# Performance work log

Measured on AMD Instinct MI355X. Metric: run time of the kernel, lower is better.

Reference implementation:

```python
import jax, jax.numpy as jnp
import numpy as np

NUM_BLOCKS = 8
D = 1024          # residual_dim == attention_dim
FF = 4096         # feed_forward_dim
B, S = 4, 4096
EPS_ATTN = 1e-6
EPS_LN = 1e-6


def _ln(x, scale, bias):
    m = jnp.mean(x, axis=-1, keepdims=True)
    v = jnp.var(x, axis=-1, keepdims=True)
    return (x - m) * jax.lax.rsqrt(v + EPS_LN) * scale + bias


def setup_inputs() -> dict:
    key = jax.random.key(0)
    ks = jax.random.split(key, 16)
    g = lambda k, shape, fan: jax.random.normal(k, shape, jnp.float32) * (1.0 / np.sqrt(fan))
    inp = {
        "x": jax.random.normal(ks[0], (B, S, D), jnp.float32),
        "Wq": g(ks[1], (NUM_BLOCKS, D, D), D), "bq": jnp.zeros((NUM_BLOCKS, D), jnp.float32),
        "Wk": g(ks[2], (NUM_BLOCKS, D, D), D), "bk": jnp.zeros((NUM_BLOCKS, D), jnp.float32),
        "Wv": g(ks[3], (NUM_BLOCKS, D, D), D), "bv": jnp.zeros((NUM_BLOCKS, D), jnp.float32),
        "Wo": g(ks[4], (NUM_BLOCKS, D, D), D), "bo": jnp.zeros((NUM_BLOCKS, D), jnp.float32),
        "ln1_s": jnp.ones((NUM_BLOCKS, D), jnp.float32), "ln1_b": jnp.zeros((NUM_BLOCKS, D), jnp.float32),
        "W1": g(ks[5], (NUM_BLOCKS, D, FF), D), "b1": jnp.zeros((NUM_BLOCKS, FF), jnp.float32),
        "W2": g(ks[6], (NUM_BLOCKS, FF, D), FF), "b2": jnp.zeros((NUM_BLOCKS, D), jnp.float32),
        "ln2_s": jnp.ones((NUM_BLOCKS, D), jnp.float32), "ln2_b": jnp.zeros((NUM_BLOCKS, D), jnp.float32),
    }
    return inp


def _forward(x, Wq, bq, Wk, bk, Wv, bv, Wo, bo, ln1_s, ln1_b, W1, b1, W2, b2, ln2_s, ln2_b):
    gelu = lambda t: jax.nn.gelu(t, approximate=True)  # flax nn.gelu default
    fmap = lambda t: jax.nn.elu(t) + 1.0
    for i in range(NUM_BLOCKS):
        # --- linear attention sublayer ---
        residual = x
        Q = fmap(x @ Wq[i] + bq[i])          # [b, s, h]
        K = fmap(x @ Wk[i] + bk[i])          # [b, s, h]
        value = x @ Wv[i] + bv[i]            # [b, s, h]
        KV = jnp.einsum('nsh,nsh->nh', K, value)          # per-channel sum_s K*V
        Ksum = jnp.sum(K, axis=1)                         # [b, h]
        Z = 1.0 / (Q * Ksum[:, None, :] + EPS_ATTN)       # [b, s, h]
        V = Q * KV[:, None, :] * Z                        # [b, s, h]
        attn_out = gelu(V @ Wo[i] + bo[i])
        x = _ln(attn_out + residual, ln1_s[i], ln1_b[i])
        # --- feed-forward sublayer ---
        residual = x
        h = gelu(x @ W1[i] + b1[i])
        ff_out = gelu(h @ W2[i] + b2[i])
        x = _ln(ff_out + residual, ln2_s[i], ln2_b[i])
    return x


def reference(x, Wq, bq, Wk, bk, Wv, bv, Wo, bo, ln1_s, ln1_b, W1, b1, W2, b2, ln2_s, ln2_b):
    return _forward(x, Wq, bq, Wk, bk, Wv, bv, Wo, bo, ln1_s, ln1_b, W1, b1, W2, b2, ln2_s, ln2_b)
```

## Files before the change

### kernel.cpp

```cpp
#include <hip/hip_runtime.h>
#include <hip/hip_bf16.h>
#include <cstdint>

typedef unsigned short ushort_t;
typedef __attribute__((ext_vector_type(8))) short short8;
typedef __attribute__((ext_vector_type(4))) float floatx4;
typedef __attribute__((ext_vector_type(4))) ushort_t ushort4v;

#define DEVI __device__ __forceinline__

DEVI float b2f(ushort_t u){ union{unsigned int i; float f;} v; v.i = ((unsigned int)u)<<16; return v.f; }
DEVI ushort_t f2b(float f){ union{float f; unsigned int i;} v; v.f=f; unsigned int r = (v.i + 0x7FFFu + ((v.i>>16)&1u)) >> 16; return (ushort_t)r; }

DEVI float gelu_f(float t){
  float t3 = t*t*t;
  return 0.5f*t*(1.0f + tanhf(0.7978845608028654f*(t + 0.044715f*t3)));
}

#define GLD_LDS16(src, dst) \
  __builtin_amdgcn_global_load_lds((const __attribute__((address_space(1))) void*)(src), \
                                   (__attribute__((address_space(3))) void*)(dst), 16, 0, 0)

template<int EPI>
__global__ __launch_bounds__(256)
void gemm_kernel(const ushort_t* __restrict__ A, const ushort_t* __restrict__ Bt,
                 const float* __restrict__ bias, const float* __restrict__ res,
                 ushort_t* __restrict__ out, int N, int K)
{
  __shared__ alignas(16) ushort_t As[2][4096];
  __shared__ alignas(16) ushort_t Bs[2][4096];
  const int tid  = threadIdx.x;
  const int wave = tid >> 6, lane = tid & 63;
  const int quad = lane >> 4, l16 = lane & 15;
  const int tileM = blockIdx.x * 128, tileN = blockIdx.y * 128;
  const int wm = (wave >> 1) * 64, wn = (wave & 1) * 64;
  const int sw = quad ^ (l16 & 3);

  floatx4 acc[4][4] = {};

  const int r0 = tid >> 2,        kd0 = (tid & 3) ^ (r0 & 3);
  const int r1 = (256+tid) >> 2,  kd1 = ((256+tid) & 3) ^ (r1 & 3);
  const size_t aoff0 = (size_t)(tileM + r0) * K + kd0 * 8;
  const size_t aoff1 = (size_t)(tileM + r1) * K + kd1 * 8;
  const size_t boff0 = (size_t)(tileN + r0) * K + kd0 * 8;
  const size_t boff1 = (size_t)(tileN + r1) * K + kd1 * 8;

  GLD_LDS16(A  + aoff0, &As[0][0] + wave*512);
  GLD_LDS16(A  + aoff1, &As[0][0] + 2048 + wave*512);
  GLD_LDS16(Bt + boff0, &Bs[0][0] + wave*512);
  GLD_LDS16(Bt + boff1, &Bs[0][0] + 2048 + wave*512);

  const int nIter = K >> 5;
  for (int it = 0; it < nIter; ++it){
    const int cur = it & 1, nxt = cur ^ 1;
    __syncthreads();
    if (it + 1 < nIter){
      const size_t k8 = (size_t)(it + 1) * 32;
      GLD_LDS16(A  + aoff0 + k8, &As[nxt][0] + wave*512);
      GLD_LDS16(A  + aoff1 + k8, &As[nxt][0] + 2048 + wave*512);
      GLD_LDS16(Bt + boff0 + k8, &Bs[nxt][0] + wave*512);
      GLD_LDS16(Bt + boff1 + k8, &Bs[nxt][0] + 2048 + wave*512);
    }
    short8 af[4], bfv[4];
    #pragma unroll
    for (int i = 0; i < 4; i++){
      af[i]  = *(const short8*)(&As[cur][0] + ((wm + i*16 + l16)*4 + sw)*8);
      bfv[i] = *(const short8*)(&Bs[cur][0] + ((wn + i*16 + l16)*4 + sw)*8);
    }
    #pragma unroll
    for (int mi = 0; mi < 4; mi++)
      #pragma unroll
      for (int ni = 0; ni < 4; ni++)
        acc[mi][ni] = __builtin_amdgcn_mfma_f32_16x16x32_bf16(af[mi], bfv[ni], acc[mi][ni], 0, 0, 0);
  }

  float bv4[4];
  #pragma unroll
  for (int ni = 0; ni < 4; ni++) bv4[ni] = bias[tileN + wn + ni*16 + l16];

  #pragma unroll
  for (int mi = 0; mi < 4; mi++){
    #pragma unroll
    for (int r = 0; r < 4; r++){
      const int row = tileM + wm + mi*16 + quad*4 + r;
      #pragma unroll
      for (int ni = 0; ni < 4; ni++){
        const int col = tileN + wn + ni*16 + l16;
        float v = acc[mi][ni][r] + bv4[ni];
        if constexpr (EPI == 0){ v = (v > 0.f) ? (v + 1.f) : expf(v); }
        else if constexpr (EPI == 2){ v = gelu_f(v); }
        else if constexpr (EPI == 3){ v = gelu_f(v) + res[(size_t)row*N + col]; }
        out[(size_t)row*N + col] = f2b(v);
      }
    }
  }
}

__global__ __launch_bounds__(256)
void qkv_gemm_kernel(const ushort_t* __restrict__ A, const ushort_t* __restrict__ Bt,
                     const float* __restrict__ bq, const float* __restrict__ bk,
                     const float* __restrict__ bv,
                     ushort_t* __restrict__ outQ, ushort_t* __restrict__ outK,
                     ushort_t* __restrict__ outV, int K)
{
  __shared__ alignas(16) ushort_t As[2][4096];
  __shared__ alignas(16) ushort_t Bs[2][4096];
  const int tid  = threadIdx.x;
  const int wave = tid >> 6, lane = tid & 63;
  const int quad = lane >> 4, l16 = lane & 15;
  const int tileM = blockIdx.x * 128, tileN = blockIdx.y * 128;
  const int wm = (wave >> 1) * 64, wn = (wave & 1) * 64;
  const int sw = quad ^ (l16 & 3);

  const int seg = tileN >> 10;
  const int nloc = tileN & 1023;
  const float* bias = (seg == 0) ? bq : (seg == 1) ? bk : bv;
  ushort_t* out     = (seg == 0) ? outQ : (seg == 1) ? outK : outV;

  floatx4 acc[4][4] = {};

  const int r0 = tid >> 2,        kd0 = (tid & 3) ^ (r0 & 3);
  const int r1 = (256+tid) >> 2,  kd1 = ((256+tid) & 3) ^ (r1 & 3);
  const size_t aoff0 = (size_t)(tileM + r0) * K + kd0 * 8;
  const size_t aoff1 = (size_t)(tileM + r1) * K + kd1 * 8;
  const size_t boff0 = (size_t)(tileN + r0) * K + kd0 * 8;
  const size_t boff1 = (size_t)(tileN + r1) * K + kd1 * 8;

  GLD_LDS16(A  + aoff0, &As[0][0] + wave*512);
  GLD_LDS16(A  + aoff1, &As[0][0] + 2048 + wave*512);
  GLD_LDS16(Bt + boff0, &Bs[0][0] + wave*512);
  GLD_LDS16(Bt + boff1, &Bs[0][0] + 2048 + wave*512);

  const int nIter = K >> 5;
  for (int it = 0; it < nIter; ++it){
    const int cur = it & 1, nxt = cur ^ 1;
    __syncthreads();
    if (it + 1 < nIter){
      const size_t k8 = (size_t)(it + 1) * 32;
      GLD_LDS16(A  + aoff0 + k8, &As[nxt][0] + wave*512);
      GLD_LDS16(A  + aoff1 + k8, &As[nxt][0] + 2048 + wave*512);
      GLD_LDS16(Bt + boff0 + k8, &Bs[nxt][0] + wave*512);
      GLD_LDS16(Bt + boff1 + k8, &Bs[nxt][0] + 2048 + wave*512);
    }
    short8 af[4], bfv[4];
    #pragma unroll
    for (int i = 0; i < 4; i++){
      af[i]  = *(const short8*)(&As[cur][0] + ((wm + i*16 + l16)*4 + sw)*8);
      bfv[i] = *(const short8*)(&Bs[cur][0] + ((wn + i*16 + l16)*4 + sw)*8);
    }
    #pragma unroll
    for (int mi = 0; mi < 4; mi++)
      #pragma unroll
      for (int ni = 0; ni < 4; ni++)
        acc[mi][ni] = __builtin_amdgcn_mfma_f32_16x16x32_bf16(af[mi], bfv[ni], acc[mi][ni], 0, 0, 0);
  }

  float bv4[4];
  #pragma unroll
  for (int ni = 0; ni < 4; ni++) bv4[ni] = bias[nloc + wn + ni*16 + l16];

  #pragma unroll
  for (int mi = 0; mi < 4; mi++){
    #pragma unroll
    for (int r = 0; r < 4; r++){
      const int row = tileM + wm + mi*16 + quad*4 + r;
      #pragma unroll
      for (int ni = 0; ni < 4; ni++){
        const int col = nloc + wn + ni*16 + l16;
        float v = acc[mi][ni][r] + bv4[ni];
        if (seg < 2){ v = (v > 0.f) ? (v + 1.f) : expf(v); }
        out[(size_t)row*1024 + col] = f2b(v);
      }
    }
  }
}

__global__ __launch_bounds__(256)
void reduce_kv_kernel(const ushort_t* __restrict__ Kb, const ushort_t* __restrict__ Vb,
                      float* __restrict__ KV, float* __restrict__ Ksum)
{
  const int b = blockIdx.x >> 6, chunk = blockIdx.x & 63;
  const int t = threadIdx.x;
  const size_t base = ((size_t)b*4096 + (size_t)chunk*64)*1024 + t*4;
  float kv[4] = {0,0,0,0}, ks[4] = {0,0,0,0};
  for (int s = 0; s < 64; s++){
    ushort4v kk = *(const ushort4v*)(Kb + base + (size_t)s*1024);
    ushort4v vv = *(const ushort4v*)(Vb + base + (size_t)s*1024);
    #pragma unroll
    for (int j = 0; j < 4; j++){ float kf = b2f(kk[j]); kv[j] += kf*b2f(vv[j]); ks[j] += kf; }
  }
  #pragma unroll
  for (int j = 0; j < 4; j++){
    atomicAdd(&KV[b*1024 + t*4 + j], kv[j]);
    atomicAdd(&Ksum[b*1024 + t*4 + j], ks[j]);
  }
}

__global__ __launch_bounds__(256)
void attn_map_kernel(ushort_t* __restrict__ Q, const float* __restrict__ KV, const float* __restrict__ Ksum)
{
  const size_t g = (size_t)blockIdx.x*256 + threadIdx.x;
  const size_t base = g*4;
  const int b  = (int)(base >> 22);
  const int h0 = (int)(base & 1023);
  ushort4v q4 = *(const ushort4v*)(Q + base);
  ushort4v o4;
  #pragma unroll
  for (int j = 0; j < 4; j++){
    float q = b2f(q4[j]);
    float v = q*KV[b*1024 + h0 + j] / (q*Ksum[b*1024 + h0 + j] + 1e-6f);
    o4[j] = f2b(v);
  }
  *(ushort4v*)(Q + base) = o4;
}

__global__ __launch_bounds__(256)
void ln_kernel(const ushort_t* __restrict__ y, const float* __restrict__ sc,
               const float* __restrict__ bi, ushort_t* __restrict__ xb, float* __restrict__ xf)
{
  const int row = blockIdx.x, t = threadIdx.x;
  const ushort_t* yr = y + (size_t)row*1024;
  ushort4v v4 = *(const ushort4v*)(yr + t*4);
  float f[4]; float s1 = 0.f, s2 = 0.f;
  #pragma unroll
  for (int j = 0; j < 4; j++){ f[j] = b2f(v4[j]); s1 += f[j]; s2 += f[j]*f[j]; }
  #pragma unroll
  for (int off = 32; off; off >>= 1){ s1 += __shfl_down(s1, off); s2 += __shfl_down(s2, off); }
  __shared__ float red[2][4];
  const int wave = t >> 6, lane = t & 63;
  if (lane == 0){ red[0][wave] = s1; red[1][wave] = s2; }
  __syncthreads();
  s1 = red[0][0] + red[0][1] + red[0][2] + red[0][3];
  s2 = red[1][0] + red[1][1] + red[1][2] + red[1][3];
  const float mean = s1 * (1.0f/1024.0f);
  const float var  = s2 * (1.0f/1024.0f) - mean*mean;
  const float inv  = rsqrtf(var + 1e-6f);
  ushort4v o4;
  #pragma unroll
  for (int j = 0; j < 4; j++){
    const int h = t*4 + j;
    const float o = (f[j] - mean)*inv*sc[h] + bi[h];
    o4[j] = f2b(o);
    xf[(size_t)row*1024 + h] = o;
  }
  *(ushort4v*)(xb + (size_t)row*1024 + t*4) = o4;
}

struct TParams { const float* src[6]; ushort_t* dst[6]; };

__global__ __launch_bounds__(256)
void transpose_all_kernel(TParams p)
{
  __shared__ float tile[32][33];
  const int id = blockIdx.x;
  int m, bx, by, R, C;
  if (id < 4096){ m = 4; int l = id;        bx = l & 127; by = l >> 7; R = 1024; C = 4096; }
  else if (id < 8192){ m = 5; int l = id - 4096; bx = l & 31; by = l >> 5; R = 4096; C = 1024; }
  else { int l = id - 8192; m = l >> 10; l &= 1023; bx = l & 31; by = l >> 5; R = 1024; C = 1024; }
  const float* in = p.src[m];
  ushort_t* out = p.dst[m];
  const int t = threadIdx.x;
  const int tx = t & 31, ty = t >> 5;
  const int rb = by*32, cb = bx*32;
  #pragma unroll
  for (int j = 0; j < 32; j += 8) tile[ty+j][tx] = in[(size_t)(rb+ty+j)*C + cb+tx];
  __syncthreads();
  #pragma unroll
  for (int j = 0; j < 32; j += 8) out[(size_t)(cb+ty+j)*R + rb+tx] = f2b(tile[tx][ty+j]);
}

__global__ __launch_bounds__(256)
void cvt_kernel(const float* __restrict__ in, ushort_t* __restrict__ out)
{
  const size_t base = ((size_t)blockIdx.x*256 + threadIdx.x)*4;
  ushort4v o4;
  #pragma unroll
  for (int j = 0; j < 4; j++) o4[j] = f2b(in[base + j]);
  *(ushort4v*)(out + base) = o4;
}

extern "C" void kernel_launch(void* const* d_in, const int* in_sizes, int n_in,
                              void* d_out, int out_size, void* d_ws, size_t ws_size,
                              hipStream_t stream)
{
  const float* x_in = (const float*)d_in[0];
  const float* Wq   = (const float*)d_in[1];
  const float* bq   = (const float*)d_in[2];
  const float* Wk   = (const float*)d_in[3];
  const float* bk   = (const float*)d_in[4];
  const float* Wv   = (const float*)d_in[5];
  const float* bv   = (const float*)d_in[6];
  const float* Wo   = (const float*)d_in[7];
  const float* bo   = (const float*)d_in[8];
  const float* ln1s = (const float*)d_in[9];
  const float* ln1b = (const float*)d_in[10];
  const float* W1   = (const float*)d_in[11];
  const float* b1   = (const float*)d_in[12];
  const float* W2   = (const float*)d_in[13];
  const float* b2   = (const float*)d_in[14];
  const float* ln2s = (const float*)d_in[15];
  const float* ln2b = (const float*)d_in[16];

  float* xf = (float*)d_out;

  char* ws = (char*)d_ws;
  const size_t MB = 1024*1024;
  ushort_t* xb     = (ushort_t*)(ws);
  char*     regB   = ws + 32*MB;
  ushort_t* bufQ   = (ushort_t*)(regB);
  ushort_t* bufK   = (ushort_t*)(regB + 32*MB);
  ushort_t* bufVal = (ushort_t*)(regB + 64*MB);
  ushort_t* bufH   = (ushort_t*)(regB);
  ushort_t* bufY   = (ushort_t*)(regB + 128*MB);
  ushort_t* WqkvT  = (ushort_t*)(ws + 192*MB);
  ushort_t* WoT    = (ushort_t*)(ws + 198*MB);
  ushort_t* W1T    = (ushort_t*)(ws + 200*MB);
  ushort_t* W2T    = (ushort_t*)(ws + 208*MB);
  float*    KV     = (float*)(ws + 216*MB);
  float*    Ksum   = (float*)(ws + 216*MB + 16*1024);

  const int M = 16384, D = 1024, FF = 4096;
  const dim3 blk(256);

  hipMemcpyAsync(xf, x_in, (size_t)M*D*sizeof(float), hipMemcpyDeviceToDevice, stream);
  cvt_kernel<<<dim3(M*D/1024), blk, 0, stream>>>(x_in, xb);

  for (int i = 0; i < 8; i++){
    TParams tp;
    tp.src[0] = Wq + (size_t)i*D*D;  tp.dst[0] = WqkvT;
    tp.src[1] = Wk + (size_t)i*D*D;  tp.dst[1] = WqkvT + 1024*1024;
    tp.src[2] = Wv + (size_t)i*D*D;  tp.dst[2] = WqkvT + 2*1024*1024;
    tp.src[3] = Wo + (size_t)i*D*D;  tp.dst[3] = WoT;
    tp.src[4] = W1 + (size_t)i*D*FF; tp.dst[4] = W1T;
    tp.src[5] = W2 + (size_t)i*FF*D; tp.dst[5] = W2T;
    transpose_all_kernel<<<dim3(12288), blk, 0, stream>>>(tp);

    qkv_gemm_kernel<<<dim3(128, 24), blk, 0, stream>>>(xb, WqkvT, bq + i*D, bk + i*D, bv + i*D,
                                                       bufQ, bufK, bufVal, D);

    hipMemsetAsync(KV, 0, 32*1024, stream);
    reduce_kv_kernel<<<dim3(256), blk, 0, stream>>>(bufK, bufVal, KV, Ksum);
    attn_map_kernel<<<dim3(16384), blk, 0, stream>>>(bufQ, KV, Ksum);

    gemm_kernel<3><<<dim3(128, 8), blk, 0, stream>>>(bufQ, WoT, bo + i*D, xf, bufVal, D, D);
    ln_kernel<<<dim3(16384), blk, 0, stream>>>(bufVal, ln1s + i*D, ln1b + i*D, xb, xf);

    gemm_kernel<2><<<dim3(128, 32), blk, 0, stream>>>(xb, W1T, b1 + i*FF, nullptr, bufH, FF, D);
    gemm_kernel<3><<<dim3(128, 8),  blk, 0, stream>>>(bufH, W2T, b2 + i*D, xf, bufY, D, FF);
    ln_kernel<<<dim3(16384), blk, 0, stream>>>(bufY, ln2s + i*D, ln2b + i*D, xb, xf);
  }
  (void)in_sizes; (void)n_in; (void)out_size; (void)ws_size;
}
```

Measured before the change: 6.651 ms.

## Use 256x256 GEMM tiles with 8 waves, BK=64 and split-phase pipelined loads

Replaces the 128x128, 4-wave, BK=32 GEMM mainloop with a shared 256x256, 8-wave core that uses 64-wide K steps and an XOR-swizzled LDS layout. Global-to-LDS loads are staged in pieces interleaved with MFMA phases, using explicit vmcnt waits, barriers and s_setprio to overlap memory with compute. The larger tile raises operand reuse and cuts global traffic per FLOP. In exchange it uses 128KB of LDS and more registers per block. The grid is smaller, so small GEMMs such as N=1024 get only 256 blocks, which can underfill the GPU.

```diff
diff --git a/kernel.cpp b/kernel.cpp
--- a/kernel.cpp
+++ b/kernel.cpp
@@ -21,155 +21,168 @@
   __builtin_amdgcn_global_load_lds((const __attribute__((address_space(1))) void*)(src), \
                                    (__attribute__((address_space(3))) void*)(dst), 16, 0, 0)
 
+#define BAR()    asm volatile("s_barrier" ::: "memory")
+#define WAITV(n) asm volatile("s_waitcnt vmcnt(" #n ")" ::: "memory")
+
+DEVI void gemm_core(const ushort_t* __restrict__ A, const ushort_t* __restrict__ Bt,
+                    int K, int tileM, int tileN, floatx4 (&acc)[8][4])
+{
+  __shared__ alignas(16) ushort_t As[2][16384];
+  __shared__ alignas(16) ushort_t Bs[2][16384];
+  const int tid  = threadIdx.x;
+  const int wave = tid >> 6, lane = tid & 63;
+  const int quad = lane >> 4, l16 = lane & 15;
+  const int wm = wave >> 2, wn = wave & 3;
+
+  const int rr = tid >> 3;
+  const int gg = (tid & 7) ^ (rr & 7);
+  const ushort_t* srcA = A  + (size_t)(tileM + rr) * K + gg * 8;
+  const ushort_t* srcB = Bt + (size_t)(tileN + rr) * K + gg * 8;
+  const size_t K64 = (size_t)K * 64;
+  ushort_t* dstA = &As[0][0] + wave * 512;
+  ushort_t* dstB = &Bs[0][0] + wave * 512;
+
+#define STAGE_R(t, r) do{ \
+    const ushort_t* s_ = (((r) < 2) ? srcA : srcB) + (size_t)(t) * 64 + (((r) & 1) ? 2*K64 : (size_t)0); \
+    ushort_t* d_ = (((r) < 2) ? dstA : dstB) + (((t) & 1) ? 16384 : 0) + (((r) & 1) ? 8192 : 0); \
+    GLD_LDS16(s_,       d_); \
+    GLD_LDS16(s_ + K64, d_ + 4096); \
+  }while(0)
+
+#define PHASE_MFMA(n0, n1) \
+    BAR(); \
+    __builtin_amdgcn_s_setprio(1); \
+    _Pragma("unroll") \
+    for (int mi = 0; mi < 8; mi++){ \
+      acc[mi][n0] = __builtin_amdgcn_mfma_f32_16x16x32_bf16(af[mi], bf0, acc[mi][n0], 0, 0, 0); \
+      acc[mi][n1] = __builtin_amdgcn_mfma_f32_16x16x32_bf16(af[mi], bf1, acc[mi][n1], 0, 0, 0); \
+    } \
+    __builtin_amdgcn_s_setprio(0); \
+    BAR()
+
+  const int nkt = K >> 6;
+  STAGE_R(0, 0); STAGE_R(0, 1); STAGE_R(0, 2); STAGE_R(0, 3);
+  if (nkt > 1){
+    STAGE_R(1, 0); STAGE_R(1, 1); STAGE_R(1, 2);
+    WAITV(6);
+  } else {
+    WAITV(0);
+  }
+  BAR();
+
+  const int s0   = (quad ^ (l16 & 7)) * 8;
+  const int aRow = (wm * 128 + l16) * 64;
+  const int bRow = (wn * 64  + l16) * 64;
+
+  for (int t = 0; t < nkt; ++t){
+    const ushort_t* as = &As[t & 1][0];
+    const ushort_t* bs = &Bs[t & 1][0];
+    if (t + 1 < nkt) STAGE_R(t + 1, 3);
+
+    short8 af[8], bf0, bf1;
+    #pragma unroll
+    for (int mi = 0; mi < 8; mi++) af[mi] = *(const short8*)(as + aRow + mi * 1024 + s0);
+    bf0 = *(const short8*)(bs + bRow + s0);
+    bf1 = *(const short8*)(bs + bRow + 1024 + s0);
+    PHASE_MFMA(0, 1);
+    bf0 = *(const short8*)(bs + bRow + 2 * 1024 + s0);
+    bf1 = *(const short8*)(bs + bRow + 3 * 1024 + s0);
+    PHASE_MFMA(2, 3);
+    {
+      const int s1 = s0 ^ 32;
+      #pragma unroll
+      for (int mi = 0; mi < 8; mi++) af[mi] = *(const short8*)(as + aRow + mi * 1024 + s1);
+      bf0 = *(const short8*)(bs + bRow + s1);
+      bf1 = *(const short8*)(bs + bRow + 1024 + s1);
+      PHASE_MFMA(0, 1);
+      bf0 = *(const short8*)(bs + bRow + 2 * 1024 + s1);
+      bf1 = *(const short8*)(bs + bRow + 3 * 1024 + s1);
+      PHASE_MFMA(2, 3);
+    }
+    if (t + 2 < nkt){
+      STAGE_R(t + 2, 0); STAGE_R(t + 2, 1); STAGE_R(t + 2, 2);
+      WAITV(6);
+      BAR();
+    } else if (t + 1 < nkt){
+      WAITV(0);
+      BAR();
+    }
+  }
+#undef STAGE_R
+#undef PHASE_MFMA
+}
+
 template<int EPI>
-__global__ __launch_bounds__(256)
+__global__ __launch_bounds__(512, 2)
 void gemm_kernel(const ushort_t* __restrict__ A, const ushort_t* __restrict__ Bt,
                  const float* __restrict__ bias, const float* __restrict__ res,
                  ushort_t* __restrict__ out, int N, int K)
 {
-  __shared__ alignas(16) ushort_t As[2][4096];
-  __shared__ alignas(16) ushort_t Bs[2][4096];
-  const int tid  = threadIdx.x;
-  const int wave = tid >> 6, lane = tid & 63;
+  const int tileM = blockIdx.x * 256, tileN = blockIdx.y * 256;
+  floatx4 acc[8][4] = {};
+  gemm_core(A, Bt, K, tileM, tileN, acc);
+
+  const int tid = threadIdx.x, wave = tid >> 6, lane = tid & 63;
   const int quad = lane >> 4, l16 = lane & 15;
-  const int tileM = blockIdx.x * 128, tileN = blockIdx.y * 128;
-  const int wm = (wave >> 1) * 64, wn = (wave & 1) * 64;
-  const int sw = quad ^ (l16 & 3);
-
-  floatx4 acc[4][4] = {};
-
-  const int r0 = tid >> 2,        kd0 = (tid & 3) ^ (r0 & 3);
-  const int r1 = (256+tid) >> 2,  kd1 = ((256+tid) & 3) ^ (r1 & 3);
-  const size_t aoff0 = (size_t)(tileM + r0) * K + kd0 * 8;
-  const size_t aoff1 = (size_t)(tileM + r1) * K + kd1 * 8;
-  const size_t boff0 = (size_t)(tileN + r0) * K + kd0 * 8;
-  const size_t boff1 = (size_t)(tileN + r1) * K + kd1 * 8;
-
-  GLD_LDS16(A  + aoff0, &As[0][0] + wave*512);
-  GLD_LDS16(A  + aoff1, &As[0][0] + 2048 + wave*512);
-  GLD_LDS16(Bt + boff0, &Bs[0][0] + wave*512);
-  GLD_LDS16(Bt + boff1, &Bs[0][0] + 2048 + wave*512);
-
-  const int nIter = K >> 5;
-  for (int it = 0; it < nIter; ++it){
-    const int cur = it & 1, nxt = cur ^ 1;
-    __syncthreads();
-    if (it + 1 < nIter){
-      const size_t k8 = (size_t)(it + 1) * 32;
-      GLD_LDS16(A  + aoff0 + k8, &As[nxt][0] + wave*512);
-      GLD_LDS16(A  + aoff1 + k8, &As[nxt][0] + 2048 + wave*512);
-      GLD_LDS16(Bt + boff0 + k8, &Bs[nxt][0] + wave*512);
-      GLD_LDS16(Bt + boff1 + k8, &Bs[nxt][0] + 2048 + wave*512);
-    }
-    short8 af[4], bfv[4];
-    #pragma unroll
-    for (int i = 0; i < 4; i++){
-      af[i]  = *(const short8*)(&As[cur][0] + ((wm + i*16 + l16)*4 + sw)*8);
-      bfv[i] = *(const short8*)(&Bs[cur][0] + ((wn + i*16 + l16)*4 + sw)*8);
-    }
-    #pragma unroll
-    for (int mi = 0; mi < 4; mi++)
-      #pragma unroll
-      for (int ni = 0; ni < 4; ni++)
-        acc[mi][ni] = __builtin_amdgcn_mfma_f32_16x16x32_bf16(af[mi], bfv[ni], acc[mi][ni], 0, 0, 0);
-  }
+  const int wm = wave >> 2, wn = wave & 3;
 
   float bv4[4];
   #pragma unroll
-  for (int ni = 0; ni < 4; ni++) bv4[ni] = bias[tileN + wn + ni*16 + l16];
-
-  #pragma unroll
-  for (int mi = 0; mi < 4; mi++){
+  for (int ni = 0; ni < 4; ni++) bv4[ni] = bias[tileN + wn * 64 + ni * 16 + l16];
+
+  #pragma unroll
+  for (int mi = 0; mi < 8; mi++){
     #pragma unroll
     for (int r = 0; r < 4; r++){
-      const int row = tileM + wm + mi*16 + quad*4 + r;
+      const int row = tileM + wm * 128 + mi * 16 + quad * 4 + r;
       #pragma unroll
       for (int ni = 0; ni < 4; ni++){
-        const int col = tileN + wn + ni*16 + l16;
+        const int col = tileN + wn * 64 + ni * 16 + l16;
         float v = acc[mi][ni][r] + bv4[ni];
         if constexpr (EPI == 0){ v = (v > 0.f) ? (v + 1.f) : expf(v); }
         else if constexpr (EPI == 2){ v = gelu_f(v); }
-        else if constexpr (EPI == 3){ v = gelu_f(v) + res[(size_t)row*N + col]; }
-        out[(size_t)row*N + col] = f2b(v);
+        else if constexpr (EPI == 3){ v = gelu_f(v) + res[(size_t)row * N + col]; }
+        out[(size_t)row * N + col] = f2b(v);
       }
     }
   }
 }
 
-__global__ __launch_bounds__(256)
+__global__ __launch_bounds__(512, 2)
 void qkv_gemm_kernel(const ushort_t* __restrict__ A, const ushort_t* __restrict__ Bt,
                      const float* __restrict__ bq, const float* __restrict__ bk,
                      const float* __restrict__ bv,
                      ushort_t* __restrict__ outQ, ushort_t* __restrict__ outK,
                      ushort_t* __restrict__ outV, int K)
 {
-  __shared__ alignas(16) ushort_t As[2][4096];
-  __shared__ alignas(16) ushort_t Bs[2][4096];
-  const int tid  = threadIdx.x;
-  const int wave = tid >> 6, lane = tid & 63;
+  const int tileM = blockIdx.x * 256, tileN = blockIdx.y * 256;
+  floatx4 acc[8][4] = {};
+  gemm_core(A, Bt, K, tileM, tileN, acc);
+
+  const int tid = threadIdx.x, wave = tid >> 6, lane = tid & 63;
   const int quad = lane >> 4, l16 = lane & 15;
-  const int tileM = blockIdx.x * 128, tileN = blockIdx.y * 128;
-  const int wm = (wave >> 1) * 64, wn = (wave & 1) * 64;
-  const int sw = quad ^ (l16 & 3);
-
-  const int seg = tileN >> 10;
+  const int wm = wave >> 2, wn = wave & 3;
+
+  const int seg  = tileN >> 10;
   const int nloc = tileN & 1023;
   const float* bias = (seg == 0) ? bq : (seg == 1) ? bk : bv;
   ushort_t* out     = (seg == 0) ? outQ : (seg == 1) ? outK : outV;
 
-  floatx4 acc[4][4] = {};
-
-  const int r0 = tid >> 2,        kd0 = (tid & 3) ^ (r0 & 3);
-  const int r1 = (256+tid) >> 2,  kd1 = ((256+tid) & 3) ^ (r1 & 3);
-  const size_t aoff0 = (size_t)(tileM + r0) * K + kd0 * 8;
-  const size_t aoff1 = (size_t)(tileM + r1) * K + kd1 * 8;
-  const size_t boff0 = (size_t)(tileN + r0) * K + kd0 * 8;
-  const size_t boff1 = (size_t)(tileN + r1) * K + kd1 * 8;
-
-  GLD_LDS16(A  + aoff0, &As[0][0] + wave*512);
-  GLD_LDS16(A  + aoff1, &As[0][0] + 2048 + wave*512);
-  GLD_LDS16(Bt + boff0, &Bs[0][0] + wave*512);
-  GLD_LDS16(Bt + boff1, &Bs[0][0] + 2048 + wave*512);
-
-  const int nIter = K >> 5;
-  for (int it = 0; it < nIter; ++it){
-    const int cur = it & 1, nxt = cur ^ 1;
-    __syncthreads();
-    if (it + 1 < nIter){
-      const size_t k8 = (size_t)(it + 1) * 32;
-      GLD_LDS16(A  + aoff0 + k8, &As[nxt][0] + wave*512);
-      GLD_LDS16(A  + aoff1 + k8, &As[nxt][0] + 2048 + wave*512);
-      GLD_LDS16(Bt + boff0 + k8, &Bs[nxt][0] + wave*512);
-      GLD_LDS16(Bt + boff1 + k8, &Bs[nxt][0] + 2048 + wave*512);
-    }
-    short8 af[4], bfv[4];
-    #pragma unroll
-    for (int i = 0; i < 4; i++){
-      af[i]  = *(const short8*)(&As[cur][0] + ((wm + i*16 + l16)*4 + sw)*8);
-      bfv[i] = *(const short8*)(&Bs[cur][0] + ((wn + i*16 + l16)*4 + sw)*8);
-    }
-    #pragma unroll
-    for (int mi = 0; mi < 4; mi++)
-      #pragma unroll
-      for (int ni = 0; ni < 4; ni++)
-        acc[mi][ni] = __builtin_amdgcn_mfma_f32_16x16x32_bf16(af[mi], bfv[ni], acc[mi][ni], 0, 0, 0);
-  }
-
   float bv4[4];
   #pragma unroll
-  for (int ni = 0; ni < 4; ni++) bv4[ni] = bias[nloc + wn + ni*16 + l16];
-
-  #pragma unroll
-  for (int mi = 0; mi < 4; mi++){
+  for (int ni = 0; ni < 4; ni++) bv4[ni] = bias[nloc + wn * 64 + ni * 16 + l16];
+
+  #pragma unroll
+  for (int mi = 0; mi < 8; mi++){
     #pragma unroll
     for (int r = 0; r < 4; r++){
-      const int row = tileM + wm + mi*16 + quad*4 + r;
+      const int row = tileM + wm * 128 + mi * 16 + quad * 4 + r;
       #pragma unroll
       for (int ni = 0; ni < 4; ni++){
-        const int col = nloc + wn + ni*16 + l16;
+        const int col = nloc + wn * 64 + ni * 16 + l16;
         float v = acc[mi][ni][r] + bv4[ni];
         if (seg < 2){ v = (v > 0.f) ? (v + 1.f) : expf(v); }
-        out[(size_t)row*1024 + col] = f2b(v);
+        out[(size_t)row * 1024 + col] = f2b(v);
       }
     }
   }
@@ -321,6 +334,7 @@
 
   const int M = 16384, D = 1024, FF = 4096;
   const dim3 blk(256);
+  const dim3 blkG(512);
 
   hipMemcpyAsync(xf, x_in, (size_t)M*D*sizeof(float), hipMemcpyDeviceToDevice, stream);
   cvt_kernel<<<dim3(M*D/1024), blk, 0, stream>>>(x_in, xb);
@@ -335,18 +349,18 @@
     tp.src[5] = W2 + (size_t)i*FF*D; tp.dst[5] = W2T;
     transpose_all_kernel<<<dim3(12288), blk, 0, stream>>>(tp);
 
-    qkv_gemm_kernel<<<dim3(128, 24), blk, 0, stream>>>(xb, WqkvT, bq + i*D, bk + i*D, bv + i*D,
+    qkv_gemm_kernel<<<dim3(64, 12), blkG, 0, stream>>>(xb, WqkvT, bq + i*D, bk + i*D, bv + i*D,
                                                        bufQ, bufK, bufVal, D);
 
     hipMemsetAsync(KV, 0, 32*1024, stream);
     reduce_kv_kernel<<<dim3(256), blk, 0, stream>>>(bufK, bufVal, KV, Ksum);
     attn_map_kernel<<<dim3(16384), blk, 0, stream>>>(bufQ, KV, Ksum);
 
-    gemm_kernel<3><<<dim3(128, 8), blk, 0, stream>>>(bufQ, WoT, bo + i*D, xf, bufVal, D, D);
+    gemm_kernel<3><<<dim3(64, 4), blkG, 0, stream>>>(bufQ, WoT, bo + i*D, xf, bufVal, D, D);
     ln_kernel<<<dim3(16384), blk, 0, stream>>>(bufVal, ln1s + i*D, ln1b + i*D, xb, xf);
 
-    gemm_kernel<2><<<dim3(128, 32), blk, 0, stream>>>(xb, W1T, b1 + i*FF, nullptr, bufH, FF, D);
-    gemm_kernel<3><<<dim3(128, 8),  blk, 0, stream>>>(bufH, W2T, b2 + i*D, xf, bufY, D, FF);
+    gemm_kernel<2><<<dim3(64, 16), blkG, 0, stream>>>(xb, W1T, b1 + i*FF, nullptr, bufH, FF, D);
+    gemm_kernel<3><<<dim3(64, 4),  blkG, 0, stream>>>(bufH, W2T, b2 + i*D, xf, bufY, D, FF);
     ln_kernel<<<dim3(16384), blk, 0, stream>>>(bufY, ln2s + i*D, ln2b + i*D, xb, xf);
   }
   (void)in_sizes; (void)n_in; (void)out_size; (void)ws_size;
```

Measured after the change: 6.403 ms. 1.04x faster.
